# Performance work log

Measured on AMD Instinct MI355X. Metric: run time of the kernel, lower is better.

The kernel has to match this reference:

```python
import jax, jax.numpy as jnp
import numpy as np

N_NODES = 50000
N_EDGES = 800000
IN_C, HID_C, OUT_C = 128, 256, 64


def _linear_params(key, fan_in, fan_out):
    kw, kb = jax.random.split(key)
    bound = 1.0 / np.sqrt(fan_in)
    w = jax.random.uniform(kw, (fan_in, fan_out), jnp.float32, -bound, bound)
    b = jax.random.uniform(kb, (fan_out,), jnp.float32, -bound, bound)
    return w, b


def setup_inputs() -> dict:
    key = jax.random.key(0)
    ks = jax.random.split(key, 8)
    x = jax.random.normal(ks[0], (N_NODES, IN_C), jnp.float32)
    edge_index = jax.random.randint(ks[1], (2, N_EDGES), 0, N_NODES, dtype=jnp.int64)
    w1a, b1a = _linear_params(ks[2], IN_C, HID_C)
    w1b, b1b = _linear_params(ks[3], HID_C, HID_C)
    w2a, b2a = _linear_params(ks[4], HID_C, HID_C)
    w2b, b2b = _linear_params(ks[5], HID_C, HID_C)
    w3a, b3a = _linear_params(ks[6], HID_C, HID_C)
    w3b, b3b = _linear_params(ks[7], HID_C, OUT_C)
    return {
        "x": x, "edge_index": edge_index,
        "w1a": w1a, "b1a": b1a, "w1b": w1b, "b1b": b1b,
        "w2a": w2a, "b2a": b2a, "w2b": w2b, "b2b": b2b,
        "w3a": w3a, "b3a": b3a, "w3b": w3b, "b3b": b3b,
    }


def _gin_conv(x, src, dst, wa, ba, wb, bb):
    # GINConv (eps=0): MLP( x + sum_{j->i} x_j )
    agg = jax.ops.segment_sum(x[src], dst, num_segments=N_NODES)  # [N, d]
    h = x + agg
    h = jnp.maximum(h @ wa + ba, 0.0)
    return h @ wb + bb


def reference(x, edge_index, w1a, b1a, w1b, b1b, w2a, b2a, w2b, b2b,
              w3a, b3a, w3b, b3b):
    src, dst = edge_index[0], edge_index[1]
    h = jnp.maximum(_gin_conv(x, src, dst, w1a, b1a, w1b, b1b), 0.0)
    h = jnp.maximum(_gin_conv(h, src, dst, w2a, b2a, w2b, b2b), 0.0)
    # output head: Linear -> ReLU -> Dropout(eval: identity) -> Linear
    h = jnp.maximum(h @ w3a + b3a, 0.0)
    return h @ w3b + b3b  # [N, OUT_C]
```

## Files before the change

kernel.cpp:

```cpp
#include <hip/hip_runtime.h>
#include <stdint.h>

#define N_NODES 50000
#define N_EDGES 800000
#define M_PAD   50048
#define NREP    4
#define MCAP    8
#define SCAP    24
#define CSTR    50048
#define LCAP    64
#define TSTR    264

typedef __attribute__((ext_vector_type(8))) short bf16x8;
typedef __attribute__((ext_vector_type(4))) float f32x4;

__device__ __forceinline__ unsigned short f2b(float f){
    unsigned int u = __builtin_bit_cast(unsigned int, f);
    u += 0x7fffu + ((u >> 16) & 1u);
    return (unsigned short)(u >> 16);
}
__device__ __forceinline__ float b2f(unsigned short s){
    unsigned int u = ((unsigned int)s) << 16;
    return __builtin_bit_cast(float, u);
}

__device__ __forceinline__ void gl_lds16(const void* g, void* l){
    __builtin_amdgcn_global_load_lds(
        (const __attribute__((address_space(1))) void*)g,
        (__attribute__((address_space(3))) void*)l, 16, 0, 0);
}

__global__ void k_x2b(const float* __restrict__ x, unsigned short* __restrict__ xs,
                      int* __restrict__ cnt){
    int gi = blockIdx.x * 256 + threadIdx.x;
    if (gi < NREP * CSTR) cnt[gi] = 0;
    size_t e0 = (size_t)gi * 8;
    if (e0 >= (size_t)M_PAD * 128) return;
    int node = (int)(e0 >> 7);
    int ch0  = (int)(e0 & 127);
    int sl = ch0 >> 5, wth = ch0 & 31;
    bf16x8 o;
    if (node < N_NODES){
        const float4* xp = (const float4*)(x + e0);
        float4 a = xp[0], b = xp[1];
        o[0] = (short)f2b(a.x); o[1] = (short)f2b(a.y);
        o[2] = (short)f2b(a.z); o[3] = (short)f2b(a.w);
        o[4] = (short)f2b(b.x); o[5] = (short)f2b(b.y);
        o[6] = (short)f2b(b.z); o[7] = (short)f2b(b.w);
    } else {
#pragma unroll
        for (int i = 0; i < 8; ++i) o[i] = 0;
    }
    *(bf16x8*)&xs[((size_t)(sl * 50048 + node)) * 32 + wth] = o;
}

__global__ void k_scatter(const int* __restrict__ ei, int* __restrict__ cnt,
                          unsigned short* __restrict__ mn, unsigned short* __restrict__ sp){
    int e = blockIdx.x * 256 + threadIdx.x;
    if (e < N_EDGES){
        unsigned d = (unsigned)ei[N_EDGES + e];
        unsigned s = (unsigned)ei[e];
        if (d < N_NODES && s < N_NODES){
            int r = threadIdx.x & 3;
            int p = atomicAdd(&cnt[r * CSTR + d], 1);
            int b = (d << 2) + r;
            if (p < MCAP) mn[(b << 3) + p] = (unsigned short)s;
            else if (p < MCAP + SCAP) sp[b * SCAP + (p - MCAP)] = (unsigned short)s;
        }
    }
}

__global__ void k_merge(const int* __restrict__ cnt, const unsigned short* __restrict__ mn,
                        const unsigned short* __restrict__ sp,
                        unsigned short* __restrict__ mg, int* __restrict__ gcnt){
    const int t = threadIdx.x;
    const int r = t & 3;
    const int n = blockIdx.x * 64 + (t >> 2);
    int c = cnt[r * CSTR + n];
    if (c > MCAP + SCAP) c = MCAP + SCAP;
    int incl = c;
    int t1 = __shfl_up(incl, 1, 4); if (r >= 1) incl += t1;
    int t2 = __shfl_up(incl, 2, 4); if (r >= 2) incl += t2;
    const int excl = incl - c;
    const int total = __shfl(incl, 3, 4);
    const unsigned mb = (unsigned)n * LCAP;
    const unsigned short* src = &mn[((n << 2) + r) << 3];
    for (int i = 0; i < c && i < MCAP; ++i){
        int pos = excl + i;
        if (pos < LCAP) mg[mb + pos] = src[i];
    }
    const unsigned short* ssrc = &sp[((n << 2) + r) * SCAP];
    for (int i = MCAP; i < c; ++i){
        int pos = excl + i;
        if (pos < LCAP) mg[mb + pos] = ssrc[i - MCAP];
    }
    if (r == 3){
        int grp = (total + 3) >> 2;
        if (grp > LCAP / 4) grp = LCAP / 4;
        gcnt[n] = grp;
        for (int pos = total; pos < grp * 4; ++pos) mg[mb + pos] = (unsigned short)N_NODES;
    }
}

template<int C, bool SPLIT>
__global__ __launch_bounds__(256) void k_aggx(const unsigned short* __restrict__ in,
        const int* __restrict__ gcnt, const unsigned short* __restrict__ mg,
        unsigned short* __restrict__ out){
    constexpr int RS = C / 8;
    const int bid = blockIdx.x, w8 = bid & 7;
    int g, nbase;
    if (SPLIT){ g = w8 & 3; nbase = ((bid >> 3) + (w8 >> 2) * 391) * 64; }
    else      { g = w8;     nbase = (bid >> 3) * 64; }
    const int lane = threadIdx.x & 63, wid = threadIdx.x >> 6;
    const int qd = lane >> 2, lq = lane & 3;
    const int n = nbase + wid * 16 + qd;
    const bf16x8* __restrict__ xr = (const bf16x8*)in;
    const unsigned sbu = (unsigned)g * 50048u;

    float a[8];
    {
        bf16x8 s = xr[(sbu + (unsigned)n) * 4u + (unsigned)lq];
#pragma unroll
        for (int i = 0; i < 8; ++i) a[i] = b2f((unsigned short)s[i]);
    }
    const int grp = gcnt[n];
    const unsigned mbase = (unsigned)n * LCAP;
    for (int k = 0; k < grp; ++k){
        ushort4 jj = *(const ushort4*)&mg[mbase + (unsigned)(k * 4)];
        unsigned i0 = (sbu + jj.x) * 4u + lq;
        unsigned i1 = (sbu + jj.y) * 4u + lq;
        unsigned i2 = (sbu + jj.z) * 4u + lq;
        unsigned i3 = (sbu + jj.w) * 4u + lq;
        bf16x8 v0 = xr[i0];
        bf16x8 v1 = xr[i1];
        bf16x8 v2 = xr[i2];
        bf16x8 v3 = xr[i3];
#pragma unroll
        for (int i = 0; i < 8; ++i)
            a[i] += (b2f((unsigned short)v0[i]) + b2f((unsigned short)v1[i]))
                  + (b2f((unsigned short)v2[i]) + b2f((unsigned short)v3[i]));
    }
    bf16x8 o;
#pragma unroll
    for (int i = 0; i < 8; ++i) o[i] = (short)f2b(a[i]);
    *(bf16x8*)&out[((unsigned)n * RS + (unsigned)(g * 4 + lq)) * 8u] = o;
}

__global__ void k_wt_all(const float* w0, const float* w1, const float* w2,
                         const float* w3, const float* w4, const float* w5,
                         unsigned short* o0, unsigned short* o1, unsigned short* o2,
                         unsigned short* o3, unsigned short* o4, unsigned short* o5){
    const int Ks[6]  = {128, 256, 256, 256, 256, 256};
    const int Ns[6]  = {256, 256, 256, 256, 256,  64};
    const int NPs[6] = {256, 256, 256, 256, 256, 128};
    int s = blockIdx.y;
    const float* w = (s == 0) ? w0 : (s == 1) ? w1 : (s == 2) ? w2
                   : (s == 3) ? w3 : (s == 4) ? w4 : w5;
    unsigned short* o = (s == 0) ? o0 : (s == 1) ? o1 : (s == 2) ? o2
                      : (s == 3) ? o3 : (s == 4) ? o4 : o5;
    int K = Ks[s], N = Ns[s], NP = NPs[s];
    int idx = blockIdx.x * 256 + threadIdx.x;
    if (idx >= NP * K) return;
    int np = idx / K, k = idx - np * K;
    float v = (np < N) ? w[(size_t)k * N + np] : 0.f;
    o[idx] = f2b(v);
}

template<int K1, int NMID, int NOUT, bool RELU_OUT, bool BF16OUT, bool SLICED>
__global__ __launch_bounds__(256) void k_mlp2(const unsigned short* __restrict__ A,
        const unsigned short* __restrict__ WA, const float* __restrict__ bA,
        const unsigned short* __restrict__ WB, const float* __restrict__ bB,
        void* __restrict__ out, int mstore){
    constexpr int NFA = NMID / 32;
    constexpr int NFB = NOUT / 32;
    __shared__ alignas(16) unsigned short As[64 * 32];
    __shared__ alignas(16) unsigned short Bs[NMID * 32];
    __shared__ alignas(16) unsigned short T[64 * TSTR];
    const int tid  = threadIdx.x;
    const int lane = tid & 63;
    const int c = lane & 15, qq = lane >> 4;
    const int kk = qq * 8;
    const int row0 = blockIdx.x * 64;
    const int wm = (tid >> 6) >> 1, wn = (tid >> 6) & 1;

    const f32x4 fzero = {0.f, 0.f, 0.f, 0.f};
    const char* Ab = (const char*)A;

    {
        f32x4 acc[NFA][2];
#pragma unroll
        for (int nf = 0; nf < NFA; ++nf){ acc[nf][0] = fzero; acc[nf][1] = fzero; }
        const char* Wb = (const char*)WA;
        for (int kt = 0; kt < K1 / 32; ++kt){
            {
                const int o = tid * 16;
                gl_lds16(Ab + ((size_t)(row0 + (o >> 6)) * K1 + kt * 32) * 2 + (o & 63),
                         (char*)As + o);
            }
#pragma unroll
            for (int ch = 0; ch < NMID / 64; ++ch){
                const int o = ch * 4096 + tid * 16;
                gl_lds16(Wb + ((size_t)(o >> 6) * K1 + kt * 32) * 2 + (o & 63),
                         (char*)Bs + o);
            }
            __syncthreads();
            bf16x8 xf[2];
#pragma unroll
            for (int mf = 0; mf < 2; ++mf)
                xf[mf] = *(const bf16x8*)&As[(wm * 32 + mf * 16 + c) * 32 + kk];
#pragma unroll
            for (int nf = 0; nf < NFA; ++nf){
                bf16x8 wf = *(const bf16x8*)&Bs[((wn * NFA + nf) * 16 + c) * 32 + kk];
#pragma unroll
                for (int mf = 0; mf < 2; ++mf)
                    acc[nf][mf] = __builtin_amdgcn_mfma_f32_16x16x32_bf16(wf, xf[mf], acc[nf][mf], 0, 0, 0);
            }
            __syncthreads();
        }
#pragma unroll
        for (int nf = 0; nf < NFA; ++nf){
            const int nb = wn * (NFA * 16) + nf * 16 + qq * 4;
            const float4 bb = *(const float4*)&bA[nb];
#pragma unroll
            for (int mf = 0; mf < 2; ++mf){
                const int ml = wm * 32 + mf * 16 + c;
                float v0 = fmaxf(acc[nf][mf][0] + bb.x, 0.f);
                float v1 = fmaxf(acc[nf][mf][1] + bb.y, 0.f);
                float v2 = fmaxf(acc[nf][mf][2] + bb.z, 0.f);
                float v3 = fmaxf(acc[nf][mf][3] + bb.w, 0.f);
                uint2 p;
                p.x = (unsigned)f2b(v0) | ((unsigned)f2b(v1) << 16);
                p.y = (unsigned)f2b(v2) | ((unsigned)f2b(v3) << 16);
                *(uint2*)&T[ml * TSTR + nb] = p;
            }
        }
    }
    __syncthreads();

    {
        f32x4 acc[NFB][2];
#pragma unroll
        for (int nf = 0; nf < NFB; ++nf){ acc[nf][0] = fzero; acc[nf][1] = fzero; }
        const char* Wb = (const char*)WB;
        for (int kt = 0; kt < NMID / 32; ++kt){
#pragma unroll
            for (int ch = 0; ch < NOUT / 64; ++ch){
                const int o = ch * 4096 + tid * 16;
                gl_lds16(Wb + ((size_t)(o >> 6) * NMID + kt * 32) * 2 + (o & 63),
                         (char*)Bs + o);
            }
            __syncthreads();
            bf16x8 xf[2];
#pragma unroll
            for (int mf = 0; mf < 2; ++mf)
                xf[mf] = *(const bf16x8*)&T[(wm * 32 + mf * 16 + c) * TSTR + kt * 32 + kk];
#pragma unroll
            for (int nf = 0; nf < NFB; ++nf){
                bf16x8 wf = *(const bf16x8*)&Bs[((wn * NFB + nf) * 16 + c) * 32 + kk];
#pragma unroll
                for (int mf = 0; mf < 2; ++mf)
                    acc[nf][mf] = __builtin_amdgcn_mfma_f32_16x16x32_bf16(wf, xf[mf], acc[nf][mf], 0, 0, 0);
            }
            __syncthreads();
        }
#pragma unroll
        for (int nf = 0; nf < NFB; ++nf){
            const int nb = wn * (NFB * 16) + nf * 16 + qq * 4;
            const float4 bb = *(const float4*)&bB[nb];
#pragma unroll
            for (int mf = 0; mf < 2; ++mf){
                const int m = row0 + wm * 32 + mf * 16 + c;
                if (m < mstore){
                    float v0 = acc[nf][mf][0] + bb.x;
                    float v1 = acc[nf][mf][1] + bb.y;
                    float v2 = acc[nf][mf][2] + bb.z;
                    float v3 = acc[nf][mf][3] + bb.w;
                    if (RELU_OUT){
                        v0 = fmaxf(v0, 0.f); v1 = fmaxf(v1, 0.f);
                        v2 = fmaxf(v2, 0.f); v3 = fmaxf(v3, 0.f);
                    }
                    if (SLICED){
                        uint2 p;
                        p.x = (unsigned)f2b(v0) | ((unsigned)f2b(v1) << 16);
                        p.y = (unsigned)f2b(v2) | ((unsigned)f2b(v3) << 16);
                        if (m >= N_NODES){ p.x = 0; p.y = 0; }
                        *(uint2*)&((unsigned short*)out)[
                            ((size_t)((nb >> 5) * 50048 + m)) * 32 + (nb & 31)] = p;
                    } else if (BF16OUT){
                        uint2 p;
                        p.x = (unsigned)f2b(v0) | ((unsigned)f2b(v1) << 16);
                        p.y = (unsigned)f2b(v2) | ((unsigned)f2b(v3) << 16);
                        *(uint2*)&((unsigned short*)out)[(size_t)m * NOUT + nb] = p;
                    } else {
                        float4 p = make_float4(v0, v1, v2, v3);
                        *(float4*)&((float*)out)[(size_t)m * NOUT + nb] = p;
                    }
                }
            }
        }
    }
}

extern "C" void kernel_launch(void* const* d_in, const int* in_sizes, int n_in,
                              void* d_out, int out_size, void* d_ws, size_t ws_size,
                              hipStream_t stream){
    const float* x   = (const float*)d_in[0];
    const int*   ei  = (const int*)d_in[1];
    const float* w1a = (const float*)d_in[2];
    const float* b1a = (const float*)d_in[3];
    const float* w1b = (const float*)d_in[4];
    const float* b1b = (const float*)d_in[5];
    const float* w2a = (const float*)d_in[6];
    const float* b2a = (const float*)d_in[7];
    const float* w2b = (const float*)d_in[8];
    const float* b2b = (const float*)d_in[9];
    const float* w3a = (const float*)d_in[10];
    const float* b3a = (const float*)d_in[11];
    const float* w3b = (const float*)d_in[12];
    const float* b3b = (const float*)d_in[13];

    char* ws = (char*)d_ws;
    size_t off = 0;
    auto take = [&](size_t bytes) -> char* {
        off = (off + 255) & ~(size_t)255;
        char* p = ws + off;
        off += bytes;
        return p;
    };
    unsigned short* xs1  = (unsigned short*)take((size_t)4 * 50048 * 32 * 2);
    unsigned short* g1   = (unsigned short*)take((size_t)M_PAD * 128 * 2);
    unsigned short* h1s  = (unsigned short*)take((size_t)8 * 50048 * 32 * 2);
    unsigned short* g2   = (unsigned short*)take((size_t)M_PAD * 256 * 2);
    unsigned short* h2   = (unsigned short*)take((size_t)M_PAD * 256 * 2);
    unsigned short* wt1a = (unsigned short*)take(256 * 128 * 2);
    unsigned short* wt1b = (unsigned short*)take(256 * 256 * 2);
    unsigned short* wt2a = (unsigned short*)take(256 * 256 * 2);
    unsigned short* wt2b = (unsigned short*)take(256 * 256 * 2);
    unsigned short* wt3a = (unsigned short*)take(256 * 256 * 2);
    unsigned short* wt3b = (unsigned short*)take(128 * 256 * 2);
    int*            cnt  = (int*)take((size_t)NREP * CSTR * 4);
    unsigned short* mn   = (unsigned short*)take((size_t)M_PAD * 4 * MCAP * 2);
    unsigned short* sp   = (unsigned short*)take((size_t)M_PAD * 4 * SCAP * 2);
    unsigned short* mg   = (unsigned short*)take((size_t)M_PAD * LCAP * 2);
    int*            gcnt = (int*)take((size_t)M_PAD * 4);

    k_x2b<<<(M_PAD * 128 / 8 + 255) / 256, 256, 0, stream>>>(x, xs1, cnt);
    k_scatter<<<(N_EDGES + 255) / 256, 256, 0, stream>>>(ei, cnt, mn, sp);
    k_merge<<<782, 256, 0, stream>>>(cnt, mn, sp, mg, gcnt);
    k_wt_all<<<dim3(256, 6), 256, 0, stream>>>(w1a, w1b, w2a, w2b, w3a, w3b,
                                               wt1a, wt1b, wt2a, wt2b, wt3a, wt3b);

    k_aggx<128, true ><<<391 * 8, 256, 0, stream>>>(xs1, gcnt, mg, g1);
    k_mlp2<128, 256, 256, true, true, true><<<M_PAD / 64, 256, 0, stream>>>(
        g1, wt1a, b1a, wt1b, b1b, h1s, M_PAD);
    k_aggx<256, false><<<782 * 8, 256, 0, stream>>>(h1s, gcnt, mg, g2);
    k_mlp2<256, 256, 256, true, true, false><<<M_PAD / 64, 256, 0, stream>>>(
        g2, wt2a, b2a, wt2b, b2b, h2, M_PAD);
    k_mlp2<256, 256, 64, false, false, false><<<M_PAD / 64, 256, 0, stream>>>(
        h2, wt3a, b3a, wt3b, b3b, d_out, N_NODES);
}
```

Before: 240.6 us.

## Compact neighbor lists with prefix-scan offsets and partition scatter by destination range

Replaces fixed 64-slot per-node neighbor lists with a compacted CSR-like layout, whose offsets come from a three-kernel prefix scan over the clamped per-node counts. Offset and group count are packed into one int that the aggregation kernels read. The scatter kernel now has each block filter edges to one of 8 destination ranges, which localizes atomics but reads edge destinations 8 times. The intent is a smaller index footprint and better locality during aggregation, at the cost of extra scan launches and redundant edge reads.

```diff
diff --git a/kernel.cpp b/kernel.cpp
--- a/kernel.cpp
+++ b/kernel.cpp
@@ -7,8 +7,9 @@
 #define NREP    4
 #define MCAP    8
 #define SCAP    24
+#define BCAP    (MCAP + SCAP)
 #define CSTR    50048
-#define LCAP    64
+#define NPX     6256
 #define TSTR    264
 
 typedef __attribute__((ext_vector_type(8))) short bf16x8;
@@ -54,57 +55,121 @@
     *(bf16x8*)&xs[((size_t)(sl * 50048 + node)) * 32 + wth] = o;
 }
 
-__global__ void k_scatter(const int* __restrict__ ei, int* __restrict__ cnt,
-                          unsigned short* __restrict__ mn, unsigned short* __restrict__ sp){
-    int e = blockIdx.x * 256 + threadIdx.x;
-    if (e < N_EDGES){
-        unsigned d = (unsigned)ei[N_EDGES + e];
-        unsigned s = (unsigned)ei[e];
-        if (d < N_NODES && s < N_NODES){
-            int r = threadIdx.x & 3;
-            int p = atomicAdd(&cnt[r * CSTR + d], 1);
-            int b = (d << 2) + r;
-            if (p < MCAP) mn[(b << 3) + p] = (unsigned short)s;
-            else if (p < MCAP + SCAP) sp[b * SCAP + (p - MCAP)] = (unsigned short)s;
-        }
-    }
-}
-
-__global__ void k_merge(const int* __restrict__ cnt, const unsigned short* __restrict__ mn,
-                        const unsigned short* __restrict__ sp,
-                        unsigned short* __restrict__ mg, int* __restrict__ gcnt){
+__global__ __launch_bounds__(256) void k_scatter(const int* __restrict__ ei,
+        int* __restrict__ cnt, unsigned short* __restrict__ mn,
+        unsigned short* __restrict__ sp){
+    const int x = blockIdx.x & 7;
+    const int c = blockIdx.x >> 3;
+    const int nlo = x * NPX, nhi = nlo + NPX;
+    const int r = threadIdx.x & 3;
+#pragma unroll
+    for (int i = 0; i < 4; ++i){
+        int e = c * 1024 + i * 256 + threadIdx.x;
+        if (e < N_EDGES){
+            int d = ei[N_EDGES + e];
+            if (d >= nlo && d < nhi && (unsigned)d < N_NODES){
+                unsigned s = (unsigned)ei[e];
+                if (s < N_NODES){
+                    int p = atomicAdd(&cnt[r * CSTR + d], 1);
+                    int b = (d << 2) + r;
+                    if (p < MCAP) mn[(b << 3) + p] = (unsigned short)s;
+                    else if (p < BCAP) sp[b * SCAP + (p - MCAP)] = (unsigned short)s;
+                }
+            }
+        }
+    }
+}
+
+__global__ void k_scan1(const int* __restrict__ cnt, int* __restrict__ bsum){
+    __shared__ int s[256];
+    int t = threadIdx.x, n = blockIdx.x * 256 + t;
+    int v = 0;
+    if (n < M_PAD){
+#pragma unroll
+        for (int r = 0; r < 4; ++r){
+            int c = cnt[r * CSTR + n];
+            v += (c > BCAP) ? BCAP : c;
+        }
+        v = (v + 3) & ~3;
+    }
+    s[t] = v;
+    __syncthreads();
+    for (int off = 128; off > 0; off >>= 1){
+        if (t < off) s[t] += s[t + off];
+        __syncthreads();
+    }
+    if (t == 0) bsum[blockIdx.x] = s[0];
+}
+
+__global__ void k_scan2(const int* __restrict__ bsum, int* __restrict__ boff){
+    __shared__ int s[256];
+    int t = threadIdx.x;
+    int v = (t < 196) ? bsum[t] : 0;
+    s[t] = v;
+    __syncthreads();
+    for (int off = 1; off < 256; off <<= 1){
+        int a = (t >= off) ? s[t - off] : 0;
+        __syncthreads();
+        s[t] += a;
+        __syncthreads();
+    }
+    boff[t] = s[t] - v;
+}
+
+__global__ void k_scan3(const int* __restrict__ cnt, const int* __restrict__ boff,
+                        int* __restrict__ mgoff){
+    __shared__ int s[256];
+    int t = threadIdx.x, n = blockIdx.x * 256 + t;
+    int v = 0;
+    if (n < M_PAD){
+#pragma unroll
+        for (int r = 0; r < 4; ++r){
+            int c = cnt[r * CSTR + n];
+            v += (c > BCAP) ? BCAP : c;
+        }
+        v = (v + 3) & ~3;
+    }
+    s[t] = v;
+    __syncthreads();
+    for (int off = 1; off < 256; off <<= 1){
+        int a = (t >= off) ? s[t - off] : 0;
+        __syncthreads();
+        s[t] += a;
+        __syncthreads();
+    }
+    if (n < M_PAD) mgoff[n] = boff[blockIdx.x] + s[t] - v;
+}
+
+__global__ void k_merge(const int* __restrict__ cnt, const int* __restrict__ mgoff,
+                        const unsigned short* __restrict__ mn, const unsigned short* __restrict__ sp,
+                        unsigned short* __restrict__ mg, int* __restrict__ mginfo){
     const int t = threadIdx.x;
     const int r = t & 3;
     const int n = blockIdx.x * 64 + (t >> 2);
     int c = cnt[r * CSTR + n];
-    if (c > MCAP + SCAP) c = MCAP + SCAP;
+    if (c > BCAP) c = BCAP;
     int incl = c;
     int t1 = __shfl_up(incl, 1, 4); if (r >= 1) incl += t1;
     int t2 = __shfl_up(incl, 2, 4); if (r >= 2) incl += t2;
     const int excl = incl - c;
     const int total = __shfl(incl, 3, 4);
-    const unsigned mb = (unsigned)n * LCAP;
+    const unsigned mb = (unsigned)mgoff[n];
     const unsigned short* src = &mn[((n << 2) + r) << 3];
-    for (int i = 0; i < c && i < MCAP; ++i){
-        int pos = excl + i;
-        if (pos < LCAP) mg[mb + pos] = src[i];
-    }
+    for (int i = 0; i < c && i < MCAP; ++i)
+        mg[mb + excl + i] = src[i];
     const unsigned short* ssrc = &sp[((n << 2) + r) * SCAP];
-    for (int i = MCAP; i < c; ++i){
-        int pos = excl + i;
-        if (pos < LCAP) mg[mb + pos] = ssrc[i - MCAP];
-    }
+    for (int i = MCAP; i < c; ++i)
+        mg[mb + excl + i] = ssrc[i - MCAP];
     if (r == 3){
         int grp = (total + 3) >> 2;
-        if (grp > LCAP / 4) grp = LCAP / 4;
-        gcnt[n] = grp;
+        mginfo[n] = ((int)mb << 6) | grp;
         for (int pos = total; pos < grp * 4; ++pos) mg[mb + pos] = (unsigned short)N_NODES;
     }
 }
 
 template<int C, bool SPLIT>
 __global__ __launch_bounds__(256) void k_aggx(const unsigned short* __restrict__ in,
-        const int* __restrict__ gcnt, const unsigned short* __restrict__ mg,
+        const int* __restrict__ mginfo, const unsigned short* __restrict__ mg,
         unsigned short* __restrict__ out){
     constexpr int RS = C / 8;
     const int bid = blockIdx.x, w8 = bid & 7;
@@ -123,18 +188,15 @@
 #pragma unroll
         for (int i = 0; i < 8; ++i) a[i] = b2f((unsigned short)s[i]);
     }
-    const int grp = gcnt[n];
-    const unsigned mbase = (unsigned)n * LCAP;
+    const int info = mginfo[n];
+    const int grp = info & 63;
+    const unsigned mbase = (unsigned)(info >> 6);
     for (int k = 0; k < grp; ++k){
         ushort4 jj = *(const ushort4*)&mg[mbase + (unsigned)(k * 4)];
-        unsigned i0 = (sbu + jj.x) * 4u + lq;
-        unsigned i1 = (sbu + jj.y) * 4u + lq;
-        unsigned i2 = (sbu + jj.z) * 4u + lq;
-        unsigned i3 = (sbu + jj.w) * 4u + lq;
-        bf16x8 v0 = xr[i0];
-        bf16x8 v1 = xr[i1];
-        bf16x8 v2 = xr[i2];
-        bf16x8 v3 = xr[i3];
+        bf16x8 v0 = xr[(sbu + jj.x) * 4u + lq];
+        bf16x8 v1 = xr[(sbu + jj.y) * 4u + lq];
+        bf16x8 v2 = xr[(sbu + jj.z) * 4u + lq];
+        bf16x8 v3 = xr[(sbu + jj.w) * 4u + lq];
 #pragma unroll
         for (int i = 0; i < 8; ++i)
             a[i] += (b2f((unsigned short)v0[i]) + b2f((unsigned short)v1[i]))
@@ -341,19 +403,25 @@
     int*            cnt  = (int*)take((size_t)NREP * CSTR * 4);
     unsigned short* mn   = (unsigned short*)take((size_t)M_PAD * 4 * MCAP * 2);
     unsigned short* sp   = (unsigned short*)take((size_t)M_PAD * 4 * SCAP * 2);
-    unsigned short* mg   = (unsigned short*)take((size_t)M_PAD * LCAP * 2);
-    int*            gcnt = (int*)take((size_t)M_PAD * 4);
+    unsigned short* mg   = (unsigned short*)take((size_t)1100000 * 2);
+    int*            mgoff  = (int*)take((size_t)M_PAD * 4);
+    int*            mginfo = (int*)take((size_t)M_PAD * 4);
+    int*            bsum = (int*)take(256 * 4);
+    int*            boff = (int*)take(256 * 4);
 
     k_x2b<<<(M_PAD * 128 / 8 + 255) / 256, 256, 0, stream>>>(x, xs1, cnt);
-    k_scatter<<<(N_EDGES + 255) / 256, 256, 0, stream>>>(ei, cnt, mn, sp);
-    k_merge<<<782, 256, 0, stream>>>(cnt, mn, sp, mg, gcnt);
+    k_scatter<<<782 * 8, 256, 0, stream>>>(ei, cnt, mn, sp);
+    k_scan1<<<196, 256, 0, stream>>>(cnt, bsum);
+    k_scan2<<<1,   256, 0, stream>>>(bsum, boff);
+    k_scan3<<<196, 256, 0, stream>>>(cnt, boff, mgoff);
+    k_merge<<<782, 256, 0, stream>>>(cnt, mgoff, mn, sp, mg, mginfo);
     k_wt_all<<<dim3(256, 6), 256, 0, stream>>>(w1a, w1b, w2a, w2b, w3a, w3b,
                                                wt1a, wt1b, wt2a, wt2b, wt3a, wt3b);
 
-    k_aggx<128, true ><<<391 * 8, 256, 0, stream>>>(xs1, gcnt, mg, g1);
+    k_aggx<128, true ><<<391 * 8, 256, 0, stream>>>(xs1, mginfo, mg, g1);
     k_mlp2<128, 256, 256, true, true, true><<<M_PAD / 64, 256, 0, stream>>>(
         g1, wt1a, b1a, wt1b, b1b, h1s, M_PAD);
-    k_aggx<256, false><<<782 * 8, 256, 0, stream>>>(h1s, gcnt, mg, g2);
+    k_aggx<256, false><<<782 * 8, 256, 0, stream>>>(h1s, mginfo, mg, g2);
     k_mlp2<256, 256, 256, true, true, false><<<M_PAD / 64, 256, 0, stream>>>(
         g2, wt2a, b2a, wt2b, b2b, h2, M_PAD);
     k_mlp2<256, 256, 64, false, false, false><<<M_PAD / 64, 256, 0, stream>>>(
```

Result: faster. 217.9 us (-9.4%).
